# Performance work log

Hardware: AMD Instinct MI355X
Metric: run time of the kernel (lower is better)

Reference implementation:

```python
import jax, jax.numpy as jnp
import numpy as np
from jax import lax

EMBED_DIM = 1024
NUM_HEADS = 8
KEY_DIM = EMBED_DIM // NUM_HEADS  # 128
B, H, W = 2, 48, 48
N = H * W


def _rope(t, sin, cos):
    # t: [..., d]; sin/cos broadcastable to t
    x1 = t[..., ::2]
    x2 = t[..., 1::2]
    rot = jnp.stack([-x2, x1], axis=-1).reshape(t.shape)  # interleave (-x2, x1)
    return t * cos - rot * sin


def setup_inputs() -> dict:
    key = jax.random.key(0)
    ks = jax.random.split(key, 16)
    C = EMBED_DIM
    w = 0.02
    return {
        "x": jax.random.normal(ks[0], (B, H, W, C), jnp.float32),
        "sin": jax.random.normal(ks[1], (H, W, KEY_DIM), jnp.float32),
        "cos": jax.random.normal(ks[2], (H, W, KEY_DIM), jnp.float32),
        "mask": jax.random.normal(ks[3], (NUM_HEADS, N, N), jnp.float32),
        "Wq": jax.random.normal(ks[4], (C, C), jnp.float32) * w,
        "bq": jax.random.normal(ks[5], (C,), jnp.float32) * w,
        "Wk": jax.random.normal(ks[6], (C, C), jnp.float32) * w,
        "bk": jax.random.normal(ks[7], (C,), jnp.float32) * w,
        "Wv": jax.random.normal(ks[8], (C, C), jnp.float32) * w,
        "bv": jax.random.normal(ks[9], (C,), jnp.float32) * w,
        "lepe_w": jax.random.normal(ks[10], (5, 5, 1, C), jnp.float32) * w,  # HWIO, groups=C
        "lepe_b": jax.random.normal(ks[11], (C,), jnp.float32) * w,
        "Wo": jax.random.normal(ks[12], (C, C), jnp.float32) * w,
        "bo": jnp.zeros((C,), jnp.float32),
    }


def reference(x, sin, cos, mask, Wq, bq, Wk, bk, Wv, bv, lepe_w, lepe_b, Wo, bo):
    Bb, Hh, Ww, C = x.shape
    nh, kd = NUM_HEADS, KEY_DIM
    scaling = kd ** -0.5

    q = x @ Wq.T + bq                     # [B,H,W,C]
    k = (x @ Wk.T + bk) * scaling         # [B,H,W,C]
    v = x @ Wv.T + bv                     # [B,H,W,C]

    # depthwise 5x5 lepe on NHWC
    lepe = lax.conv_general_dilated(
        v, lepe_w, window_strides=(1, 1), padding="SAME",
        dimension_numbers=("NHWC", "HWIO", "NHWC"),
        feature_group_count=C,
    ) + lepe_b

    # [B,H,W,C] -> [B,nh,H,W,kd]
    qh = q.reshape(Bb, Hh, Ww, nh, kd).transpose(0, 3, 1, 2, 4)
    kh = k.reshape(Bb, Hh, Ww, nh, kd).transpose(0, 3, 1, 2, 4)

    sin_ = sin[None, None]  # [1,1,H,W,kd]
    cos_ = cos[None, None]
    qh = _rope(qh, sin_, cos_)
    kh = _rope(kh, sin_, cos_)

    qf = qh.reshape(Bb, nh, Hh * Ww, kd)  # [B,nh,N,kd]
    kf = kh.reshape(Bb, nh, Hh * Ww, kd)
    vf = v.reshape(Bb, Hh, Ww, nh, kd).transpose(0, 3, 1, 2, 4).reshape(Bb, nh, Hh * Ww, kd)

    attn = jnp.einsum("bhnd,bhmd->bhnm", qf, kf) + mask  # [B,nh,N,N]
    attn = jax.nn.softmax(attn, axis=-1)
    out = jnp.einsum("bhnm,bhmd->bhnd", attn, vf)         # [B,nh,N,kd]

    out = out.transpose(0, 2, 1, 3).reshape(Bb, Hh, Ww, nh * kd)
    out = out + lepe
    return out @ Wo.T + bo
```

## Files before the change

kernel.cpp:

```cpp
#include <hip/hip_runtime.h>
#include <hip/hip_bf16.h>
#include <stdint.h>

typedef __bf16 bf16_t;
typedef __bf16 bf16x8 __attribute__((ext_vector_type(8)));
typedef __bf16 bf16x4 __attribute__((ext_vector_type(4)));
typedef float f32x4 __attribute__((ext_vector_type(4)));
typedef unsigned int u32x4 __attribute__((ext_vector_type(4)));

#define MFMA16(A, B, C) __builtin_amdgcn_mfma_f32_16x16x32_bf16(A, B, C, 0, 0, 0)

__device__ inline void dma16(const void* g, void* l) {
    __builtin_amdgcn_global_load_lds(
        (const __attribute__((address_space(1))) unsigned int*)g,
        (__attribute__((address_space(3))) unsigned int*)l, 16, 0, 0);
}

__device__ inline unsigned pack2(float a, float b) {
    unsigned short ua = __builtin_bit_cast(unsigned short, (bf16_t)a);
    unsigned short ub = __builtin_bit_cast(unsigned short, (bf16_t)b);
    return (unsigned)ua | ((unsigned)ub << 16);
}

__global__ __launch_bounds__(256)
void cvt_kernel(const float* __restrict__ in, bf16_t* __restrict__ outp, int n8)
{
    int i = blockIdx.x * 256 + threadIdx.x;
    if (i >= n8) return;
    const float* p = in + (size_t)i * 8;
    f32x4 a = *(const f32x4*)p;
    f32x4 b = *(const f32x4*)(p + 4);
    bf16x8 r;
    r[0] = (bf16_t)a[0]; r[1] = (bf16_t)a[1]; r[2] = (bf16_t)a[2]; r[3] = (bf16_t)a[3];
    r[4] = (bf16_t)b[0]; r[5] = (bf16_t)b[1]; r[6] = (bf16_t)b[2]; r[7] = (bf16_t)b[3];
    *(bf16x8*)(outp + (size_t)i * 8) = r;
}

__global__ __launch_bounds__(256)
void cvt4_kernel(const float* __restrict__ W0, const float* __restrict__ W1,
                 const float* __restrict__ W2, const float* __restrict__ W3,
                 bf16_t* __restrict__ outp)
{
    int i = blockIdx.x * 256 + threadIdx.x;
    int sel = i >> 17;
    int j = i & 131071;
    const float* src = sel == 0 ? W0 : sel == 1 ? W1 : sel == 2 ? W2 : W3;
    const float* p = src + (size_t)j * 8;
    f32x4 a = *(const f32x4*)p;
    f32x4 b = *(const f32x4*)(p + 4);
    bf16x8 r;
    r[0] = (bf16_t)a[0]; r[1] = (bf16_t)a[1]; r[2] = (bf16_t)a[2]; r[3] = (bf16_t)a[3];
    r[4] = (bf16_t)b[0]; r[5] = (bf16_t)b[1]; r[6] = (bf16_t)b[2]; r[7] = (bf16_t)b[3];
    *(bf16x8*)(outp + (size_t)i * 8) = r;
}

__device__ __forceinline__
void gemm_core64(const bf16_t* __restrict__ A, const bf16_t* __restrict__ W,
                 const float* __restrict__ bias, void* __restrict__ outp,
                 int mode, float scale,
                 const float* __restrict__ sinp, const float* __restrict__ cosp,
                 int m0, int n0, char* lds)
{
    const int K = 1024;
    const int ASZ = 8192, BUF = 24576;
    const int t = threadIdx.x;
    const int w = t >> 6, l = t & 63;
    const int wm = w >> 1, wn = w & 1;
    const int lr = l & 15;
    const int kch = (l >> 4) * 8;

    const f32x4 zz = {0.f, 0.f, 0.f, 0.f};
    f32x4 acc[2][4];
#pragma unroll
    for (int i = 0; i < 2; i++)
#pragma unroll
        for (int j = 0; j < 4; j++) acc[i][j] = zz;

#define GSTAGE(base, kk)                                                        \
    {                                                                           \
        int a0 = w * 2;                                                         \
        dma16(A + (size_t)(m0 + (a0 >> 1) * 16 + lr) * K + (kk) + (a0 & 1) * 32 + kch, \
              (base) + a0 * 1024);                                              \
        int a1 = w * 2 + 1;                                                     \
        dma16(A + (size_t)(m0 + (a1 >> 1) * 16 + lr) * K + (kk) + (a1 & 1) * 32 + kch, \
              (base) + a1 * 1024);                                              \
        _Pragma("unroll")                                                       \
        for (int i = 0; i < 4; i++) {                                           \
            int f = w * 4 + i;                                                  \
            dma16(W + (size_t)(n0 + (f >> 1) * 16 + lr) * K + (kk) + (f & 1) * 32 + kch, \
                  (base) + ASZ + f * 1024);                                     \
        }                                                                       \
    }

    GSTAGE(lds, 0);
    __syncthreads();

    int bo = 0;
    for (int k0 = 0; k0 < K; k0 += 64) {
        int kn = k0 + 64;
        if (kn < K) {
            char* nb = lds + (bo ^ BUF);
            GSTAGE(nb, kn);
        }
#pragma unroll
        for (int kh = 0; kh < 2; kh++) {
            bf16x8 af[2], bfg[4];
#pragma unroll
            for (int mt = 0; mt < 2; mt++)
                af[mt] = *(const bf16x8*)(lds + bo + (((wm * 2 + mt) * 2 + kh) * 64 + l) * 16);
#pragma unroll
            for (int nt = 0; nt < 4; nt++)
                bfg[nt] = *(const bf16x8*)(lds + bo + ASZ + (((wn * 4 + nt) * 2 + kh) * 64 + l) * 16);
#pragma unroll
            for (int mt = 0; mt < 2; mt++)
#pragma unroll
                for (int nt = 0; nt < 4; nt++)
                    acc[mt][nt] = MFMA16(af[mt], bfg[nt], acc[mt][nt]);
        }
        __syncthreads();
        bo ^= BUF;
    }
#undef GSTAGE

    const int quad = l >> 4, lc = l & 15;
#pragma unroll
    for (int mt = 0; mt < 2; mt++) {
#pragma unroll
        for (int nt = 0; nt < 4; nt++) {
            int gn = n0 + wn * 64 + nt * 16 + lc;
            float bv = bias[gn];
            int gm0 = m0 + wm * 32 + mt * 16 + quad * 4;
            if (mode == 0) {
                float* o32 = (float*)outp;
#pragma unroll
                for (int r = 0; r < 4; r++)
                    o32[(size_t)(gm0 + r) * 1024 + gn] = acc[mt][nt][r] + bv;
            } else if (mode == 1) {
                bf16_t* ob = (bf16_t*)outp;
                int h = gn >> 7, d = gn & 127;
#pragma unroll
                for (int r = 0; r < 4; r++) {
                    int gm = gm0 + r;
                    int b = gm / 2304;
                    int pos = gm - b * 2304;
                    float val = acc[mt][nt][r] + bv;
                    float pv = __shfl_xor(val, 1);
                    float sn = sinp[pos * 128 + d];
                    float cs = cosp[pos * 128 + d];
                    float res = (d & 1) ? (val * cs - pv * sn) : (val * cs + pv * sn);
                    ob[(((size_t)b * 8 + h) * 2304 + pos) * 128 + d] = (bf16_t)(res * scale);
                }
            } else {
                bf16_t* ob = (bf16_t*)outp;
                int h = gn >> 7, d = gn & 127;
                int b = gm0 / 2304;
                int pos0 = gm0 - b * 2304;
                bf16x4 s4;
#pragma unroll
                for (int r = 0; r < 4; r++)
                    s4[r] = (bf16_t)(acc[mt][nt][r] + bv);
                *(bf16x4*)(ob + (((size_t)b * 8 + h) * 128 + d) * 2304 + pos0) = s4;
            }
        }
    }
}

__global__ __launch_bounds__(256)
void gemm_bt_kernel(const bf16_t* __restrict__ A, const bf16_t* __restrict__ W,
                    const float* __restrict__ bias, void* __restrict__ outp,
                    int mode, float scale,
                    const float* __restrict__ sinp, const float* __restrict__ cosp)
{
    __shared__ __align__(16) char lds[49152];
    gemm_core64(A, W, bias, outp, mode, scale, sinp, cosp,
                blockIdx.x * 64, blockIdx.y * 128, lds);
}

__global__ __launch_bounds__(256)
void gemm_qkv_kernel(const bf16_t* __restrict__ A, const bf16_t* __restrict__ Wall,
                     const float* __restrict__ bq, const float* __restrict__ bk,
                     const float* __restrict__ bv,
                     void* __restrict__ qb, void* __restrict__ kb, void* __restrict__ vtb,
                     const float* __restrict__ sinp, const float* __restrict__ cosp,
                     float kscale)
{
    __shared__ __align__(16) char lds[49152];
    int ny = blockIdx.y;
    int third = ny >> 3;
    int n0 = (ny & 7) * 128;
    const bf16_t* W = Wall + (size_t)third * 1048576;
    const float* bias = third == 0 ? bq : third == 1 ? bk : bv;
    void* outp = third == 0 ? qb : third == 1 ? kb : vtb;
    int mode = third == 2 ? 2 : 1;
    float scale = third == 1 ? kscale : 1.0f;
    gemm_core64(A, W, bias, outp, mode, scale, sinp, cosp, blockIdx.x * 64, n0, lds);
}

__global__ __launch_bounds__(256, 2)
void attn_kernel(const bf16_t* __restrict__ q, const bf16_t* __restrict__ k,
                 const bf16_t* __restrict__ vt, const float* __restrict__ mask,
                 bf16_t* __restrict__ o)
{
    const int N = 2304;
    const int HK = 1152;
    __shared__ __align__(16) char lds[65536];

    const int t = threadIdx.x;
    const int w = t >> 6, l = t & 63;
    const int hv = w >> 1, wl = w & 1;
    const int quad = l >> 4, lc = l & 15;

    int gid = blockIdx.x;
    int grp = gid >> 4, sub = gid & 15;
    int u = grp * 8 + (sub & 7);
    int b = sub >> 3;
    int qblk = u >> 3, h = u & 7;
    int bh = b * 8 + h;
    int q0 = qblk * 64;

    int qrow0 = q0 + wl * 32 + lc;
    int qrow1 = qrow0 + 16;

    const bf16_t* qb = q + (size_t)bh * N * 128;
    const bf16_t* kb = k + (size_t)bh * N * 128 + (size_t)hv * HK * 128;
    const bf16_t* vtb = vt + (size_t)bh * 128 * N + hv * HK;
    const float* mq0 = mask + (size_t)h * N * N + (size_t)qrow0 * N + hv * HK + quad * 4;
    const float* mq1 = mq0 + (size_t)16 * N;

    char* Ks = lds + hv * 32768;
    char* Vts = Ks + 16384;

    bf16x8 qf[2][4];
#pragma unroll
    for (int kc = 0; kc < 4; kc++) {
        qf[0][kc] = *(const bf16x8*)(qb + (size_t)qrow0 * 128 + kc * 32 + quad * 8);
        qf[1][kc] = *(const bf16x8*)(qb + (size_t)qrow1 * 128 + kc * 32 + quad * 8);
    }

    const f32x4 zz = {0.f, 0.f, 0.f, 0.f};
    float Mr0 = -1e30f, Mr1 = -1e30f, Lr0 = 0.f, Lr1 = 0.f;
    f32x4 Oacc[2][8];
#pragma unroll
    for (int fr = 0; fr < 2; fr++)
#pragma unroll
        for (int i = 0; i < 8; i++) Oacc[fr][i] = zz;

    for (int kv0 = 0; kv0 < HK; kv0 += 64) {
        __syncthreads();
#pragma unroll
        for (int i = 0; i < 8; i++) {
            int f = wl * 8 + i;
            dma16(kb + (size_t)(kv0 + (f >> 2) * 16 + lc) * 128 + (f & 3) * 32 + quad * 8,
                  Ks + f * 1024);
            dma16(vtb + (size_t)((f >> 1) * 16 + lc) * N + kv0 + (f & 1) * 32 + quad * 8,
                  Vts + f * 1024);
        }
        __syncthreads();

        f32x4 mv0[4], mv1[4];
#pragma unroll
        for (int nt = 0; nt < 4; nt++) {
            mv0[nt] = *(const f32x4*)(mq0 + kv0 + nt * 16);
            mv1[nt] = *(const f32x4*)(mq1 + kv0 + nt * 16);
        }

        f32x4 s0[4], s1[4];
#pragma unroll
        for (int nt = 0; nt < 4; nt++) {
            f32x4 a0 = zz, a1 = zz;
#pragma unroll
            for (int kc = 0; kc < 4; kc++) {
                bf16x8 kf = *(const bf16x8*)(Ks + ((nt * 4 + kc) * 64 + l) * 16);
                a0 = MFMA16(kf, qf[0][kc], a0);
                a1 = MFMA16(kf, qf[1][kc], a1);
            }
            s0[nt] = a0 + mv0[nt];
            s1[nt] = a1 + mv1[nt];
        }

        float mx0 = fmaxf(fmaxf(fmaxf(s0[0][0], s0[0][1]), fmaxf(s0[0][2], s0[0][3])),
                          fmaxf(fmaxf(s0[1][0], s0[1][1]), fmaxf(s0[1][2], s0[1][3])));
        mx0 = fmaxf(mx0, fmaxf(fmaxf(fmaxf(s0[2][0], s0[2][1]), fmaxf(s0[2][2], s0[2][3])),
                               fmaxf(fmaxf(s0[3][0], s0[3][1]), fmaxf(s0[3][2], s0[3][3]))));
        float mx1 = fmaxf(fmaxf(fmaxf(s1[0][0], s1[0][1]), fmaxf(s1[0][2], s1[0][3])),
                          fmaxf(fmaxf(s1[1][0], s1[1][1]), fmaxf(s1[1][2], s1[1][3])));
        mx1 = fmaxf(mx1, fmaxf(fmaxf(fmaxf(s1[2][0], s1[2][1]), fmaxf(s1[2][2], s1[2][3])),
                               fmaxf(fmaxf(s1[3][0], s1[3][1]), fmaxf(s1[3][2], s1[3][3]))));
        mx0 = fmaxf(mx0, __shfl_xor(mx0, 16));
        mx1 = fmaxf(mx1, __shfl_xor(mx1, 16));
        mx0 = fmaxf(mx0, __shfl_xor(mx0, 32));
        mx1 = fmaxf(mx1, __shfl_xor(mx1, 32));

        int small = (mx0 <= Mr0 + 8.f) && (mx1 <= Mr1 + 8.f);
        float al0 = 1.f, al1 = 1.f;
        if (!__all(small)) {
            float mn0 = fmaxf(Mr0, mx0), mn1 = fmaxf(Mr1, mx1);
            al0 = __expf(Mr0 - mn0);
            al1 = __expf(Mr1 - mn1);
            Mr0 = mn0; Mr1 = mn1;
#pragma unroll
            for (int dt = 0; dt < 8; dt++)
#pragma unroll
                for (int r = 0; r < 4; r++) {
                    Oacc[0][dt][r] *= al0;
                    Oacc[1][dt][r] *= al1;
                }
        }

        float rs0 = 0.f, rs1 = 0.f;
        unsigned pw0[4][2], pw1[4][2];
#pragma unroll
        for (int nt = 0; nt < 4; nt++) {
            float p0 = __expf(s0[nt][0] - Mr0);
            float p1 = __expf(s0[nt][1] - Mr0);
            float p2 = __expf(s0[nt][2] - Mr0);
            float p3 = __expf(s0[nt][3] - Mr0);
            float t0 = __expf(s1[nt][0] - Mr1);
            float t1 = __expf(s1[nt][1] - Mr1);
            float t2 = __expf(s1[nt][2] - Mr1);
            float t3 = __expf(s1[nt][3] - Mr1);
            rs0 += (p0 + p1) + (p2 + p3);
            rs1 += (t0 + t1) + (t2 + t3);
            pw0[nt][0] = pack2(p0, p1);
            pw0[nt][1] = pack2(p2, p3);
            pw1[nt][0] = pack2(t0, t1);
            pw1[nt][1] = pack2(t2, t3);
        }
        rs0 += __shfl_xor(rs0, 16);
        rs1 += __shfl_xor(rs1, 16);
        rs0 += __shfl_xor(rs0, 32);
        rs1 += __shfl_xor(rs1, 32);
        Lr0 = Lr0 * al0 + rs0;
        Lr1 = Lr1 * al1 + rs1;

#pragma unroll
        for (int pc = 0; pc < 2; pc++) {
            u32x4 wv0, wv1;
#pragma unroll
            for (int jp = 0; jp < 4; jp++) {
                int src = ((quad & 1) * 2 + (jp >> 1)) * 16 + lc;
                int a0 = __shfl((int)pw0[pc * 2 + 0][jp & 1], src);
                int a1 = __shfl((int)pw0[pc * 2 + 1][jp & 1], src);
                int c0 = __shfl((int)pw1[pc * 2 + 0][jp & 1], src);
                int c1 = __shfl((int)pw1[pc * 2 + 1][jp & 1], src);
                wv0[jp] = (quad >> 1) ? (unsigned)a1 : (unsigned)a0;
                wv1[jp] = (quad >> 1) ? (unsigned)c1 : (unsigned)c0;
            }
            bf16x8 pf0 = __builtin_bit_cast(bf16x8, wv0);
            bf16x8 pf1 = __builtin_bit_cast(bf16x8, wv1);
#pragma unroll
            for (int dt = 0; dt < 8; dt++) {
                bf16x8 vf = *(const bf16x8*)(Vts + ((dt * 2 + pc) * 64 + l) * 16);
                Oacc[0][dt] = MFMA16(vf, pf0, Oacc[0][dt]);
                Oacc[1][dt] = MFMA16(vf, pf1, Oacc[1][dt]);
            }
        }
    }

    __syncthreads();
    float* Ml = (float*)(lds + 32768);
    if (hv == 1) {
        float* ob = (float*)lds;
#pragma unroll
        for (int fr = 0; fr < 2; fr++)
#pragma unroll
            for (int dt = 0; dt < 8; dt++)
                *(f32x4*)(ob + (size_t)(((wl * 2 + fr) * 8 + dt) * 64 + l) * 4) = Oacc[fr][dt];
        if (quad == 0) {
            Ml[wl * 32 + lc]       = Mr0;
            Ml[wl * 32 + 16 + lc]  = Mr1;
            Ml[128 + wl * 32 + lc]      = Lr0;
            Ml[128 + wl * 32 + 16 + lc] = Lr1;
        }
    }
    __syncthreads();
    if (hv == 0) {
        const float* ob = (const float*)lds;
#pragma unroll
        for (int fr = 0; fr < 2; fr++) {
            float Mh = fr ? Mr1 : Mr0;
            float Lh = fr ? Lr1 : Lr0;
            int qrow = fr ? qrow1 : qrow0;
            float M1 = Ml[wl * 32 + fr * 16 + lc];
            float L1 = Ml[128 + wl * 32 + fr * 16 + lc];
            float M = fmaxf(Mh, M1);
            float w0 = __expf(Mh - M), w1 = __expf(M1 - M);
            float inv = 1.f / (Lh * w0 + L1 * w1);
#pragma unroll
            for (int dt = 0; dt < 8; dt++) {
                f32x4 o1 = *(const f32x4*)(ob + (size_t)(((wl * 2 + fr) * 8 + dt) * 64 + l) * 4);
                bf16x4 s4;
#pragma unroll
                for (int r = 0; r < 4; r++)
                    s4[r] = (bf16_t)((Oacc[fr][dt][r] * w0 + o1[r] * w1) * inv);
                *(bf16x4*)(o + ((size_t)b * N + qrow) * 1024 + h * 128 + dt * 16 + quad * 4) = s4;
            }
        }
    }
}

__global__ __launch_bounds__(256)
void lepe_kernel(const bf16_t* __restrict__ vt, const float* __restrict__ wgt,
                 const float* __restrict__ lb, const bf16_t* __restrict__ o,
                 bf16_t* __restrict__ ab)
{
    __shared__ __align__(16) bf16_t sv[5 * 48 * 128];
    const int bh = blockIdx.y;
    const int b = bh >> 3, h = bh & 7;
    const int y0 = blockIdx.x;
    const int t = threadIdx.x;

#pragma unroll
    for (int it = 0; it < 15; it++) {
        int idx = t + it * 256;
        int ck = idx % 6;
        int dy = idx / 6;
        int d = dy & 127, yloc = dy >> 7;
        int y = y0 - 2 + yloc;
        bf16x8 vvv;
#pragma unroll
        for (int j = 0; j < 8; j++) vvv[j] = (bf16_t)0.f;
        if (y >= 0 && y < 48)
            vvv = *(const bf16x8*)(vt + ((size_t)bh * 128 + d) * 2304 + y * 48 + ck * 8);
        int x0 = ck * 8;
#pragma unroll
        for (int j = 0; j < 8; j++)
            sv[(yloc * 48 + x0 + j) * 128 + d] = vvv[j];
    }
    __syncthreads();

    const int d0 = (t & 15) * 8;
    const int xb = t >> 4;
    float acc[3][8];
    f32x4 b0 = *(const f32x4*)(lb + h * 128 + d0);
    f32x4 b1 = *(const f32x4*)(lb + h * 128 + d0 + 4);
#pragma unroll
    for (int c = 0; c < 3; c++)
#pragma unroll
        for (int j = 0; j < 4; j++) { acc[c][j] = b0[j]; acc[c][4 + j] = b1[j]; }

#pragma unroll
    for (int ky = 0; ky < 5; ky++) {
#pragma unroll
        for (int kx = 0; kx < 5; kx++) {
            const float* wp = wgt + (size_t)(ky * 5 + kx) * 1024 + h * 128 + d0;
            f32x4 w0 = *(const f32x4*)wp;
            f32x4 w1 = *(const f32x4*)(wp + 4);
#pragma unroll
            for (int c = 0; c < 3; c++) {
                int xx = xb + c * 16 + kx - 2;
                if (xx < 0 || xx >= 48) continue;
                bf16x8 vv = *(const bf16x8*)(&sv[(ky * 48 + xx) * 128 + d0]);
#pragma unroll
                for (int j = 0; j < 4; j++) {
                    acc[c][j]     += (float)vv[j]     * w0[j];
                    acc[c][4 + j] += (float)vv[4 + j] * w1[j];
                }
            }
        }
    }
#pragma unroll
    for (int c = 0; c < 3; c++) {
        int x = xb + c * 16;
        size_t off = ((size_t)b * 2304 + y0 * 48 + x) * 1024 + h * 128 + d0;
        bf16x8 ov = *(const bf16x8*)(o + off);
        bf16x8 res;
#pragma unroll
        for (int j = 0; j < 8; j++) res[j] = (bf16_t)(acc[c][j] + (float)ov[j]);
        *(bf16x8*)(ab + off) = res;
    }
}

extern "C" void kernel_launch(void* const* d_in, const int* in_sizes, int n_in,
                              void* d_out, int out_size, void* d_ws, size_t ws_size,
                              hipStream_t stream)
{
    const float* x    = (const float*)d_in[0];
    const float* sin_ = (const float*)d_in[1];
    const float* cos_ = (const float*)d_in[2];
    const float* mask = (const float*)d_in[3];
    const float* Wq   = (const float*)d_in[4];
    const float* bq   = (const float*)d_in[5];
    const float* Wk   = (const float*)d_in[6];
    const float* bk   = (const float*)d_in[7];
    const float* Wv   = (const float*)d_in[8];
    const float* bv   = (const float*)d_in[9];
    const float* lw   = (const float*)d_in[10];
    const float* lb   = (const float*)d_in[11];
    const float* Wo   = (const float*)d_in[12];
    const float* bo   = (const float*)d_in[13];

    const size_t NB = (size_t)2 * 2304 * 1024;

    bf16_t* dout_b = (bf16_t*)d_out;
    bf16_t* x16 = dout_b;
    bf16_t* vtb = dout_b + NB;
    bf16_t* ob  = dout_b;

    bf16_t* qb   = (bf16_t*)d_ws;
    bf16_t* kb   = qb + NB;
    bf16_t* wbuf = kb + NB;
    bf16_t* ab   = qb;

    dim3 blk(256);
    const float kscale = 0.08838834764831845f;

    cvt_kernel<<<2304, blk, 0, stream>>>(x, x16, 589824);
    cvt4_kernel<<<2048, blk, 0, stream>>>(Wq, Wk, Wv, Wo, wbuf);
    gemm_qkv_kernel<<<dim3(72, 24), blk, 0, stream>>>(x16, wbuf, bq, bk, bv,
                                                      qb, kb, vtb, sin_, cos_, kscale);
    attn_kernel<<<576, blk, 0, stream>>>(qb, kb, vtb, mask, ob);
    lepe_kernel<<<dim3(48, 16), blk, 0, stream>>>(vtb, lw, lb, ob, ab);
    gemm_bt_kernel<<<dim3(72, 8), blk, 0, stream>>>(ab, wbuf + 3 * 1048576, bo,
                                                    d_out, 0, 1.0f, nullptr, nullptr);
}
```

Before: 596.4 us.

## Enlarge GEMM tiles to 128x128, load attention K/V straight to registers

The GEMM core now computes 128x128 output tiles with a 32-wide K step and a smaller double buffer, which halves the grid for the QKV and output projections and gives more MFMA work per LDS fragment. The attention kernel drops its LDS staging of K and V tiles and the two block-wide barriers per KV step. Each wave now loads K and V fragments directly from global memory into registers, and setprio hints are wrapped around the MFMA bursts. This removes sync and LDS traffic but raises register pressure and relies on the cache for the repeated global K/V reads. The smaller grid may also leave some CUs underused.

```diff
diff --git a/kernel.cpp b/kernel.cpp
--- a/kernel.cpp
+++ b/kernel.cpp
@@ -55,14 +55,13 @@
 }
 
 __device__ __forceinline__
-void gemm_core64(const bf16_t* __restrict__ A, const bf16_t* __restrict__ W,
-                 const float* __restrict__ bias, void* __restrict__ outp,
-                 int mode, float scale,
-                 const float* __restrict__ sinp, const float* __restrict__ cosp,
-                 int m0, int n0, char* lds)
+void gemm_core(const bf16_t* __restrict__ A, const bf16_t* __restrict__ W,
+               const float* __restrict__ bias, void* __restrict__ outp,
+               int mode, float scale,
+               const float* __restrict__ sinp, const float* __restrict__ cosp,
+               int m0, int n0, char* lds)
 {
     const int K = 1024;
-    const int ASZ = 8192, BUF = 24576;
     const int t = threadIdx.x;
     const int w = t >> 6, l = t & 63;
     const int wm = w >> 1, wn = w & 1;
@@ -70,66 +69,56 @@
     const int kch = (l >> 4) * 8;
 
     const f32x4 zz = {0.f, 0.f, 0.f, 0.f};
-    f32x4 acc[2][4];
-#pragma unroll
-    for (int i = 0; i < 2; i++)
+    f32x4 acc[4][4];
+#pragma unroll
+    for (int i = 0; i < 4; i++)
 #pragma unroll
         for (int j = 0; j < 4; j++) acc[i][j] = zz;
 
-#define GSTAGE(base, kk)                                                        \
-    {                                                                           \
-        int a0 = w * 2;                                                         \
-        dma16(A + (size_t)(m0 + (a0 >> 1) * 16 + lr) * K + (kk) + (a0 & 1) * 32 + kch, \
-              (base) + a0 * 1024);                                              \
-        int a1 = w * 2 + 1;                                                     \
-        dma16(A + (size_t)(m0 + (a1 >> 1) * 16 + lr) * K + (kk) + (a1 & 1) * 32 + kch, \
-              (base) + a1 * 1024);                                              \
-        _Pragma("unroll")                                                       \
-        for (int i = 0; i < 4; i++) {                                           \
-            int f = w * 4 + i;                                                  \
-            dma16(W + (size_t)(n0 + (f >> 1) * 16 + lr) * K + (kk) + (f & 1) * 32 + kch, \
-                  (base) + ASZ + f * 1024);                                     \
-        }                                                                       \
-    }
-
-    GSTAGE(lds, 0);
+#pragma unroll
+    for (int i = 0; i < 2; i++) {
+        int f = w * 2 + i;
+        dma16(A + (size_t)(m0 + f * 16 + lr) * K + kch, lds + f * 1024);
+        dma16(W + (size_t)(n0 + f * 16 + lr) * K + kch, lds + 8192 + f * 1024);
+    }
     __syncthreads();
 
     int bo = 0;
-    for (int k0 = 0; k0 < K; k0 += 64) {
-        int kn = k0 + 64;
+    for (int k0 = 0; k0 < K; k0 += 32) {
+        int kn = k0 + 32;
         if (kn < K) {
-            char* nb = lds + (bo ^ BUF);
-            GSTAGE(nb, kn);
-        }
-#pragma unroll
-        for (int kh = 0; kh < 2; kh++) {
-            bf16x8 af[2], bfg[4];
-#pragma unroll
-            for (int mt = 0; mt < 2; mt++)
-                af[mt] = *(const bf16x8*)(lds + bo + (((wm * 2 + mt) * 2 + kh) * 64 + l) * 16);
+            int nb = bo ^ 16384;
+#pragma unroll
+            for (int i = 0; i < 2; i++) {
+                int f = w * 2 + i;
+                dma16(A + (size_t)(m0 + f * 16 + lr) * K + kn + kch, lds + nb + f * 1024);
+                dma16(W + (size_t)(n0 + f * 16 + lr) * K + kn + kch, lds + nb + 8192 + f * 1024);
+            }
+        }
+        bf16x8 af[4], bfg[4];
+#pragma unroll
+        for (int mt = 0; mt < 4; mt++)
+            af[mt] = *(const bf16x8*)(lds + bo + ((wm * 4 + mt) * 64 + l) * 16);
+#pragma unroll
+        for (int nt = 0; nt < 4; nt++)
+            bfg[nt] = *(const bf16x8*)(lds + bo + 8192 + ((wn * 4 + nt) * 64 + l) * 16);
+#pragma unroll
+        for (int mt = 0; mt < 4; mt++)
 #pragma unroll
             for (int nt = 0; nt < 4; nt++)
-                bfg[nt] = *(const bf16x8*)(lds + bo + ASZ + (((wn * 4 + nt) * 2 + kh) * 64 + l) * 16);
-#pragma unroll
-            for (int mt = 0; mt < 2; mt++)
-#pragma unroll
-                for (int nt = 0; nt < 4; nt++)
-                    acc[mt][nt] = MFMA16(af[mt], bfg[nt], acc[mt][nt]);
-        }
+                acc[mt][nt] = MFMA16(af[mt], bfg[nt], acc[mt][nt]);
         __syncthreads();
-        bo ^= BUF;
-    }
-#undef GSTAGE
+        bo ^= 16384;
+    }
 
     const int quad = l >> 4, lc = l & 15;
 #pragma unroll
-    for (int mt = 0; mt < 2; mt++) {
+    for (int mt = 0; mt < 4; mt++) {
 #pragma unroll
         for (int nt = 0; nt < 4; nt++) {
             int gn = n0 + wn * 64 + nt * 16 + lc;
             float bv = bias[gn];
-            int gm0 = m0 + wm * 32 + mt * 16 + quad * 4;
+            int gm0 = m0 + wm * 64 + mt * 16 + quad * 4;
             if (mode == 0) {
                 float* o32 = (float*)outp;
 #pragma unroll
@@ -171,9 +160,9 @@
                     int mode, float scale,
                     const float* __restrict__ sinp, const float* __restrict__ cosp)
 {
-    __shared__ __align__(16) char lds[49152];
-    gemm_core64(A, W, bias, outp, mode, scale, sinp, cosp,
-                blockIdx.x * 64, blockIdx.y * 128, lds);
+    __shared__ __align__(16) char lds[32768];
+    gemm_core(A, W, bias, outp, mode, scale, sinp, cosp,
+              blockIdx.x * 128, blockIdx.y * 128, lds);
 }
 
 __global__ __launch_bounds__(256)
@@ -184,7 +173,7 @@
                      const float* __restrict__ sinp, const float* __restrict__ cosp,
                      float kscale)
 {
-    __shared__ __align__(16) char lds[49152];
+    __shared__ __align__(16) char lds[32768];
     int ny = blockIdx.y;
     int third = ny >> 3;
     int n0 = (ny & 7) * 128;
@@ -193,7 +182,7 @@
     void* outp = third == 0 ? qb : third == 1 ? kb : vtb;
     int mode = third == 2 ? 2 : 1;
     float scale = third == 1 ? kscale : 1.0f;
-    gemm_core64(A, W, bias, outp, mode, scale, sinp, cosp, blockIdx.x * 64, n0, lds);
+    gemm_core(A, W, bias, outp, mode, scale, sinp, cosp, blockIdx.x * 128, n0, lds);
 }
 
 __global__ __launch_bounds__(256, 2)
@@ -203,11 +192,11 @@
 {
     const int N = 2304;
     const int HK = 1152;
-    __shared__ __align__(16) char lds[65536];
+    __shared__ __align__(16) char lds[33792];
 
     const int t = threadIdx.x;
     const int w = t >> 6, l = t & 63;
-    const int hv = w >> 1, wl = w & 1;
+    const int hv = w >> 1, r2 = w & 1;
     const int quad = l >> 4, lc = l & 15;
 
     int gid = blockIdx.x;
@@ -218,17 +207,14 @@
     int bh = b * 8 + h;
     int q0 = qblk * 64;
 
-    int qrow0 = q0 + wl * 32 + lc;
+    int qrow0 = q0 + r2 * 32 + lc;
     int qrow1 = qrow0 + 16;
 
-    const bf16_t* qb = q + (size_t)bh * N * 128;
-    const bf16_t* kb = k + (size_t)bh * N * 128 + (size_t)hv * HK * 128;
-    const bf16_t* vtb = vt + (size_t)bh * 128 * N + hv * HK;
-    const float* mq0 = mask + (size_t)h * N * N + (size_t)qrow0 * N + hv * HK + quad * 4;
+    const bf16_t* qb  = q  + (size_t)bh * N * 128;
+    const bf16_t* kbp = k  + (size_t)bh * N * 128;
+    const bf16_t* vtp = vt + (size_t)bh * 128 * N;
+    const float* mq0 = mask + (size_t)h * N * N + (size_t)qrow0 * N + quad * 4;
     const float* mq1 = mq0 + (size_t)16 * N;
-
-    char* Ks = lds + hv * 32768;
-    char* Vts = Ks + 16384;
 
     bf16x8 qf[2][4];
 #pragma unroll
@@ -245,18 +231,15 @@
 #pragma unroll
         for (int i = 0; i < 8; i++) Oacc[fr][i] = zz;
 
-    for (int kv0 = 0; kv0 < HK; kv0 += 64) {
-        __syncthreads();
-#pragma unroll
-        for (int i = 0; i < 8; i++) {
-            int f = wl * 8 + i;
-            dma16(kb + (size_t)(kv0 + (f >> 2) * 16 + lc) * 128 + (f & 3) * 32 + quad * 8,
-                  Ks + f * 1024);
-            dma16(vtb + (size_t)((f >> 1) * 16 + lc) * N + kv0 + (f & 1) * 32 + quad * 8,
-                  Vts + f * 1024);
-        }
-        __syncthreads();
-
+    const int kvbeg = hv * HK, kvend = kvbeg + HK;
+    for (int kv0 = kvbeg; kv0 < kvend; kv0 += 64) {
+        bf16x8 kf[4][4];
+#pragma unroll
+        for (int nt = 0; nt < 4; nt++)
+#pragma unroll
+            for (int kc = 0; kc < 4; kc++)
+                kf[nt][kc] = *(const bf16x8*)(kbp + (size_t)(kv0 + nt * 16 + lc) * 128
+                                              + kc * 32 + quad * 8);
         f32x4 mv0[4], mv1[4];
 #pragma unroll
         for (int nt = 0; nt < 4; nt++) {
@@ -265,18 +248,27 @@
         }
 
         f32x4 s0[4], s1[4];
+        __builtin_amdgcn_s_setprio(1);
 #pragma unroll
         for (int nt = 0; nt < 4; nt++) {
             f32x4 a0 = zz, a1 = zz;
 #pragma unroll
             for (int kc = 0; kc < 4; kc++) {
-                bf16x8 kf = *(const bf16x8*)(Ks + ((nt * 4 + kc) * 64 + l) * 16);
-                a0 = MFMA16(kf, qf[0][kc], a0);
-                a1 = MFMA16(kf, qf[1][kc], a1);
+                a0 = MFMA16(kf[nt][kc], qf[0][kc], a0);
+                a1 = MFMA16(kf[nt][kc], qf[1][kc], a1);
             }
             s0[nt] = a0 + mv0[nt];
             s1[nt] = a1 + mv1[nt];
         }
+        __builtin_amdgcn_s_setprio(0);
+
+        bf16x8 vf[8][2];
+#pragma unroll
+        for (int dt = 0; dt < 8; dt++)
+#pragma unroll
+            for (int pc = 0; pc < 2; pc++)
+                vf[dt][pc] = *(const bf16x8*)(vtp + (size_t)(dt * 16 + lc) * N
+                                              + kv0 + pc * 32 + quad * 8);
 
         float mx0 = fmaxf(fmaxf(fmaxf(s0[0][0], s0[0][1]), fmaxf(s0[0][2], s0[0][3])),
                           fmaxf(fmaxf(s0[1][0], s0[1][1]), fmaxf(s0[1][2], s0[1][3])));
@@ -348,12 +340,13 @@
             }
             bf16x8 pf0 = __builtin_bit_cast(bf16x8, wv0);
             bf16x8 pf1 = __builtin_bit_cast(bf16x8, wv1);
+            __builtin_amdgcn_s_setprio(1);
 #pragma unroll
             for (int dt = 0; dt < 8; dt++) {
-                bf16x8 vf = *(const bf16x8*)(Vts + ((dt * 2 + pc) * 64 + l) * 16);
-                Oacc[0][dt] = MFMA16(vf, pf0, Oacc[0][dt]);
-                Oacc[1][dt] = MFMA16(vf, pf1, Oacc[1][dt]);
-            }
+                Oacc[0][dt] = MFMA16(vf[dt][pc], pf0, Oacc[0][dt]);
+                Oacc[1][dt] = MFMA16(vf[dt][pc], pf1, Oacc[1][dt]);
+            }
+            __builtin_amdgcn_s_setprio(0);
         }
     }
 
@@ -365,12 +358,12 @@
         for (int fr = 0; fr < 2; fr++)
 #pragma unroll
             for (int dt = 0; dt < 8; dt++)
-                *(f32x4*)(ob + (size_t)(((wl * 2 + fr) * 8 + dt) * 64 + l) * 4) = Oacc[fr][dt];
+                *(f32x4*)(ob + (size_t)(((r2 * 2 + fr) * 8 + dt) * 64 + l) * 4) = Oacc[fr][dt];
         if (quad == 0) {
-            Ml[wl * 32 + lc]       = Mr0;
-            Ml[wl * 32 + 16 + lc]  = Mr1;
-            Ml[128 + wl * 32 + lc]      = Lr0;
-            Ml[128 + wl * 32 + 16 + lc] = Lr1;
+            Ml[r2 * 32 + lc]            = Mr0;
+            Ml[r2 * 32 + 16 + lc]       = Mr1;
+            Ml[128 + r2 * 32 + lc]      = Lr0;
+            Ml[128 + r2 * 32 + 16 + lc] = Lr1;
         }
     }
     __syncthreads();
@@ -381,14 +374,14 @@
             float Mh = fr ? Mr1 : Mr0;
             float Lh = fr ? Lr1 : Lr0;
             int qrow = fr ? qrow1 : qrow0;
-            float M1 = Ml[wl * 32 + fr * 16 + lc];
-            float L1 = Ml[128 + wl * 32 + fr * 16 + lc];
+            float M1 = Ml[r2 * 32 + fr * 16 + lc];
+            float L1 = Ml[128 + r2 * 32 + fr * 16 + lc];
             float M = fmaxf(Mh, M1);
             float w0 = __expf(Mh - M), w1 = __expf(M1 - M);
             float inv = 1.f / (Lh * w0 + L1 * w1);
 #pragma unroll
             for (int dt = 0; dt < 8; dt++) {
-                f32x4 o1 = *(const f32x4*)(ob + (size_t)(((wl * 2 + fr) * 8 + dt) * 64 + l) * 4);
+                f32x4 o1 = *(const f32x4*)(ob + (size_t)(((r2 * 2 + fr) * 8 + dt) * 64 + l) * 4);
                 bf16x4 s4;
 #pragma unroll
                 for (int r = 0; r < 4; r++)
@@ -507,10 +500,10 @@
 
     cvt_kernel<<<2304, blk, 0, stream>>>(x, x16, 589824);
     cvt4_kernel<<<2048, blk, 0, stream>>>(Wq, Wk, Wv, Wo, wbuf);
-    gemm_qkv_kernel<<<dim3(72, 24), blk, 0, stream>>>(x16, wbuf, bq, bk, bv,
+    gemm_qkv_kernel<<<dim3(36, 24), blk, 0, stream>>>(x16, wbuf, bq, bk, bv,
                                                       qb, kb, vtb, sin_, cos_, kscale);
     attn_kernel<<<576, blk, 0, stream>>>(qb, kb, vtb, mask, ob);
     lepe_kernel<<<dim3(48, 16), blk, 0, stream>>>(vtb, lw, lb, ob, ab);
-    gemm_bt_kernel<<<dim3(72, 8), blk, 0, stream>>>(ab, wbuf + 3 * 1048576, bo,
+    gemm_bt_kernel<<<dim3(36, 8), blk, 0, stream>>>(ab, wbuf + 3 * 1048576, bo,
                                                     d_out, 0, 1.0f, nullptr, nullptr);
 }
```

After: 623.0 us. +4.5%, slower.
